# Kernel tuning notes

Hardware: AMD Instinct MI355X
Metric: run time of the kernel (lower is better)

Reference implementation:

```python
import jax, jax.numpy as jnp
import numpy as np

TOPK = 64
MAX_STEP = 3


def gru_cell(x, h, wih, whh, bih, bhh):
    # torch.nn.GRUCell math
    gi = x @ wih.T + bih
    gh = h @ whh.T + bhh
    i_r, i_z, i_n = jnp.split(gi, 3, axis=-1)
    h_r, h_z, h_n = jnp.split(gh, 3, axis=-1)
    r = jax.nn.sigmoid(i_r + h_r)
    z = jax.nn.sigmoid(i_z + h_z)
    n = jnp.tanh(i_n + r * h_n)
    return (1.0 - z) * n + z * h


def t_gruq_forward(query_head, support_rel_all, cos_rel_all, edge_matrix, rel_w, wih, whh, bih, bhh):
    B = query_head.shape[0]
    E = rel_w.shape[1]
    sub_cos = cos_rel_all[support_rel_all]  # [S, R] relation-score rows for support rels

    tree_node_list, tree_node_emb = [], []
    parent_index_list, parent_node_list = [], []
    rel_all_list, rel_b_list = [], []

    current = query_head[:, None]  # [B, 1]
    for step in range(1, MAX_STEP + 1):
        cand = edge_matrix[current]              # [B, nc, nei, 2]
        cand_ent = cand[..., 0]                  # [B, nc, nei]
        cand_rel = cand[..., 1]
        nc, nei = cand_ent.shape[1], cand_ent.shape[2]

        # max over support relations of cos_rel_all[s, r]
        score = sub_cos[:, cand_rel].max(axis=0)           # [B, nc, nei]
        flat = score.reshape(B, -1)                        # [B, nc*nei]
        k = min(TOPK, flat.shape[-1])
        next_scores, next_act = jax.lax.top_k(flat, k)     # [B, k]

        # parent = ceil((next_act+1)/nei) - 1 == next_act // nei
        parent = next_act // nei                           # [B, k]
        aim_ent = jnp.take_along_axis(cand_ent.reshape(B, -1), next_act, axis=1)
        aim_rel = jnp.take_along_axis(cand_rel.reshape(B, -1), next_act, axis=1)
        rel_b_list.append(aim_rel)

        x = rel_w[aim_rel].reshape(-1, E)                  # [B*k, E]
        if step == 1:
            h = jnp.zeros_like(x)
            parent_node_list.append(jnp.broadcast_to(query_head[:, None], (B, k)))
        else:
            h = jnp.take_along_axis(tree_node_emb[step - 2], parent[:, :, None], axis=1).reshape(-1, E)
            parent_node_list.append(jnp.take_along_axis(tree_node_list[step - 2], parent, axis=1))
            parent_index_list.append(parent.astype(jnp.float32))
            rel_all_list.append(jnp.take_along_axis(rel_b_list[step - 2], parent, axis=1))
            if step == MAX_STEP:
                parent_index_list.append(jnp.broadcast_to(jnp.arange(k, dtype=jnp.float32)[None, :], (B, k)))
                rel_all_list.append(aim_rel)
        emb = gru_cell(x, h, wih, whh, bih, bhh).reshape(B, k, E)
        tree_node_emb.append(emb)
        tree_node_list.append(aim_ent)
        current = aim_ent

    tree_node = jnp.stack(tree_node_list, axis=1)          # [B, 3, k]
    tree_emb_all = jnp.stack(tree_node_emb, axis=1)        # [B, 3, k, E]
    parent_index = jnp.stack(parent_index_list, axis=1)    # [B, 3, k]
    parent_node = jnp.stack(parent_node_list, axis=1)      # [B, 3, k]
    aim_rel_all = jnp.stack(rel_all_list, axis=1)          # [B, 3, k]
    return tree_node, tree_emb_all, parent_index, parent_node, aim_rel_all


def setup_inputs() -> dict:
    key = jax.random.key(0)
    ks = jax.random.split(key, 9)
    B, N_ENT, NEI, R, E, S = 512, 50000, 64, 200, 128, 16
    return {
        "query_head": jax.random.randint(ks[0], (B,), 0, N_ENT, dtype=jnp.int32),
        "support_rel_all": jax.random.randint(ks[1], (S,), 0, R, dtype=jnp.int32),
        "cos_rel_all": jax.random.normal(ks[2], (R, R), dtype=jnp.float32),
        "edge_matrix": jax.random.randint(ks[3], (N_ENT, NEI, 2), 0, R, dtype=jnp.int32),
        "rel_w": jax.random.normal(ks[4], (R, E), dtype=jnp.float32) * 0.1,
        "wih": jax.random.normal(ks[5], (3 * E, E), dtype=jnp.float32) * 0.1,
        "whh": jax.random.normal(ks[6], (3 * E, E), dtype=jnp.float32) * 0.1,
        "bih": jax.random.normal(ks[7], (3 * E,), dtype=jnp.float32) * 0.1,
        "bhh": jax.random.normal(ks[8], (3 * E,), dtype=jnp.float32) * 0.1,
    }


def reference(query_head, support_rel_all, cos_rel_all, edge_matrix, rel_w, wih, whh, bih, bhh):
    return t_gruq_forward(query_head, support_rel_all, cos_rel_all, edge_matrix, rel_w, wih, whh, bih, bhh)
```

## Files before the change

kernel.cpp:

```cpp
#include <hip/hip_runtime.h>
#include <hip/hip_bf16.h>
#include <math.h>

#define E 128
#define NEI 64
#define THREE_E 384
#define H2BS 136

typedef __attribute__((ext_vector_type(8))) short short8;
typedef __attribute__((ext_vector_type(4))) short short4v;
typedef __attribute__((ext_vector_type(4))) float f32x4;

__device__ __forceinline__ float sig_(float x) { return 1.0f / (1.0f + __expf(-x)); }
__device__ __forceinline__ float tanh_(float x) {
    float ax = fabsf(x);
    float e = __expf(-2.0f * ax);
    float r = (1.0f - e) / (1.0f + e);
    return copysignf(r, x);
}
__device__ __forceinline__ short bf16_(float x) {
    __hip_bfloat16 h = __float2bfloat16(x);
    return __builtin_bit_cast(short, h);
}

__global__ __launch_bounds__(512) void kAB(
    const int* __restrict__ support, const float* __restrict__ cosr,
    int* __restrict__ rank, int S, int R,
    const float* __restrict__ rel_w, const float* __restrict__ wih,
    const float* __restrict__ bih, float* __restrict__ G,
    const float* __restrict__ whh, const float* __restrict__ bhh,
    float* __restrict__ emb1, float* __restrict__ GH1,
    short* __restrict__ wpack) {
    int blk = blockIdx.x, t = threadIdx.x;
    __shared__ float sm[256];
    __shared__ float grow[THREE_E];
    if (blk < R) {
        int r = blk;
        if (t < E) sm[t] = rel_w[(size_t)r * E + t];
        __syncthreads();
        if (t < THREE_E) {
            float acc = bih[t];
            const float4* w4 = (const float4*)(wih + (size_t)t * E);
#pragma unroll 8
            for (int k = 0; k < E / 4; ++k) {
                float4 wv = w4[k];
                acc += sm[4 * k] * wv.x + sm[4 * k + 1] * wv.y + sm[4 * k + 2] * wv.z +
                       sm[4 * k + 3] * wv.w;
            }
            G[(size_t)r * THREE_E + t] = acc;
            grow[t] = acc;
        }
        __syncthreads();
        if (t < E) {
            float rr = sig_(grow[t] + bhh[t]);
            float zz = sig_(grow[E + t] + bhh[E + t]);
            float nn = tanh_(grow[2 * E + t] + rr * bhh[2 * E + t]);
            float h = (1.0f - zz) * nn;
            sm[t] = h;
            emb1[(size_t)r * E + t] = h;
        }
        __syncthreads();
        if (t < THREE_E) {
            float acc = bhh[t];
            const float4* w4 = (const float4*)(whh + (size_t)t * E);
#pragma unroll 8
            for (int k = 0; k < E / 4; ++k) {
                float4 wv = w4[k];
                acc += sm[4 * k] * wv.x + sm[4 * k + 1] * wv.y + sm[4 * k + 2] * wv.z +
                       sm[4 * k + 3] * wv.w;
            }
            GH1[(size_t)r * THREE_E + t] = acc;
        }
    } else if (blk < R + 96) {
        int idx = (blk - R) * 512 + t;
        int i = idx & 7, l = (idx >> 3) & 63, kt = (idx >> 9) & 3, ct = idx >> 11;
        int er = ct * 16 + (l & 15);
        int k = kt * 32 + (l >> 4) * 8 + i;
        wpack[idx] = bf16_(whh[(size_t)er * E + k]);
    } else {
        if (t < 256) {
            float v = -INFINITY;
            if (t < R)
                for (int s = 0; s < S; ++s) v = fmaxf(v, cosr[support[s] * R + t]);
            sm[t] = v;
        }
        __syncthreads();
        if (t < 256) {
            int rk = 0;
            if (t < R) {
                float v = sm[t];
                for (int r2 = 0; r2 < R; ++r2) {
                    float u = sm[r2];
                    rk += (u > v) || (u == v && r2 < t);
                }
            }
            rank[t] = rk;
        }
    }
}

__global__ __launch_bounds__(512, 6) void k_main(
    const int* __restrict__ query, const int2* __restrict__ edge,
    const int* __restrict__ rank, const float* __restrict__ G,
    const float* __restrict__ GH1, const float* __restrict__ emb1,
    const short* __restrict__ wpack, const float* __restrict__ bhh,
    float* __restrict__ o_tree, float* __restrict__ o_emb,
    float* __restrict__ o_pidx, float* __restrict__ o_pnode,
    float* __restrict__ o_rel) {
    int b = blockIdx.x, t = threadIdx.x;
    __shared__ int rankL[256];
    __shared__ int pe[64], prl[64], npe[64], nprl[64];
    __shared__ int hist[256];
    __shared__ int list[4096];
    __shared__ int win_p[64], win_rel[64], win_prel[64];
    __shared__ int s_c, s_lcnt;
    __shared__ __align__(16) short h2b[64][H2BS];

    const int* edge_i = (const int*)edge;
    if (t < 256) rankL[t] = rank[t];
    int qh = query[b];
    int e1x = 0, e1y = 0;
    if (t < 64) {
        int2 pr = edge[(size_t)qh * NEI + t];
        e1x = pr.x; e1y = pr.y;
    }
    __syncthreads();
    if (t < 64) list[t] = rankL[e1y] * 64 + t;
    __syncthreads();
    if (t < 64) {
        int mykey = list[t], pos = 0;
#pragma unroll
        for (int u = 0; u < 64; ++u) pos += (list[u] < mykey);
        pe[pos] = e1x;
        prl[pos] = e1y;
    }
    if (t < 256) hist[t] = 0;
    if (t == 0) s_lcnt = 0;
    __syncthreads();

    int p0 = t >> 6, n0 = t & 63;
    int rl2[8];
#pragma unroll
    for (int u = 0; u < 8; ++u)
        rl2[u] = edge_i[((size_t)pe[p0 + 8 * u] * NEI + n0) * 2 + 1];
    if (t < 64) {
        o_tree[(b * 3 + 0) * 64 + t] = (float)pe[t];
        o_pnode[(b * 3 + 0) * 64 + t] = (float)qh;
    }
    {
        int j = t >> 3, q = t & 7;
        const float4* src = (const float4*)(emb1 + (size_t)prl[j] * E) + q * 4;
        float4* dst = (float4*)(o_emb + ((size_t)(b * 3 + 0) * 64 + j) * E) + q * 4;
#pragma unroll
        for (int v = 0; v < 4; ++v) dst[v] = src[v];
    }
#pragma unroll
    for (int u = 0; u < 8; ++u) {
        rl2[u] = rankL[rl2[u]];
        atomicAdd(&hist[rl2[u]], 1);
    }
    __syncthreads();
    if (t < 64) {
        int base = 0, c = 255;
        for (int r4 = 0; r4 < 4; ++r4) {
            int sc = hist[r4 * 64 + t];
#pragma unroll
            for (int d = 1; d < 64; d <<= 1) {
                int o = __shfl_up(sc, d, 64);
                if (t >= d) sc += o;
            }
            unsigned long long m = __ballot(base + sc >= 64);
            if (m) { c = r4 * 64 + __ffsll(m) - 1; break; }
            base += __shfl(sc, 63, 64);
        }
        if (t == 0) s_c = c;
    }
    __syncthreads();
    {
        int c = s_c;
#pragma unroll
        for (int u = 0; u < 8; ++u)
            if (rl2[u] <= c) {
                int pos = atomicAdd(&s_lcnt, 1);
                list[pos] = (rl2[u] << 12) | (t + 512 * u);
            }
    }
    __syncthreads();
    int lcnt = s_lcnt;
    if (t < 8 && lcnt + t < 4096) list[lcnt + t] = 0x7fffffff;
    if (t < 256) hist[t] = 0;
    __syncthreads();
    {
        int lp = (lcnt + 7) & ~7;
        for (int e = t; e < lcnt; e += 512) {
            int key = list[e], ord = 0;
            for (int f = 0; f < lp; f += 8)
#pragma unroll
                for (int g = 0; g < 8; ++g) ord += (list[f + g] < key);
            if (ord < 64) {
                int i = key & 4095, p = i >> 6, n = i & 63;
                int2 c2 = edge[(size_t)pe[p] * NEI + n];
                win_rel[ord] = c2.y; win_p[ord] = p; win_prel[ord] = prl[p];
                npe[ord] = c2.x; nprl[ord] = c2.y;
                o_tree[(b * 3 + 1) * 64 + ord] = (float)c2.x;
                o_pnode[(b * 3 + 1) * 64 + ord] = (float)pe[p];
                o_pidx[(b * 3 + 0) * 64 + ord] = (float)p;
                o_rel[(b * 3 + 0) * 64 + ord] = (float)prl[p];
            }
        }
    }
    if (t == 0) s_lcnt = 0;
    __syncthreads();

    int rl3[8];
#pragma unroll
    for (int u = 0; u < 8; ++u)
        rl3[u] = edge_i[((size_t)npe[p0 + 8 * u] * NEI + n0) * 2 + 1];

    {
        int j = t >> 3, q = t & 7;
        int rel = win_rel[j], pr = win_prel[j];
        const float4* Gr = (const float4*)(G + (size_t)rel * THREE_E);
        const float4* Hr = (const float4*)(GH1 + (size_t)pr * THREE_E);
        const float4* h1 = (const float4*)(emb1 + (size_t)pr * E);
        float4* dstg = (float4*)(o_emb + ((size_t)(b * 3 + 1) * 64 + j) * E);
#pragma unroll
        for (int v = 0; v < 4; ++v) {
            int cv = q * 4 + v;
            float4 gr = Gr[cv], gz = Gr[32 + cv], gn = Gr[64 + cv];
            float4 hr = Hr[cv], hz = Hr[32 + cv], hn = Hr[64 + cv];
            float4 h = h1[cv];
            float4 res;
            { float rr = sig_(gr.x + hr.x), zz = sig_(gz.x + hz.x);
              float nn = tanh_(gn.x + rr * hn.x); res.x = (1.0f - zz) * nn + zz * h.x; }
            { float rr = sig_(gr.y + hr.y), zz = sig_(gz.y + hz.y);
              float nn = tanh_(gn.y + rr * hn.y); res.y = (1.0f - zz) * nn + zz * h.y; }
            { float rr = sig_(gr.z + hr.z), zz = sig_(gz.z + hz.z);
              float nn = tanh_(gn.z + rr * hn.z); res.z = (1.0f - zz) * nn + zz * h.z; }
            { float rr = sig_(gr.w + hr.w), zz = sig_(gz.w + hz.w);
              float nn = tanh_(gn.w + rr * hn.w); res.w = (1.0f - zz) * nn + zz * h.w; }
            dstg[cv] = res;
            short4v hb = {bf16_(res.x), bf16_(res.y), bf16_(res.z), bf16_(res.w)};
            *(short4v*)&h2b[j][cv * 4] = hb;
        }
    }
#pragma unroll
    for (int u = 0; u < 8; ++u) {
        rl3[u] = rankL[rl3[u]];
        atomicAdd(&hist[rl3[u]], 1);
    }
    __syncthreads();
    if (t < 64) {
        int base = 0, c = 255;
        for (int r4 = 0; r4 < 4; ++r4) {
            int sc = hist[r4 * 64 + t];
#pragma unroll
            for (int d = 1; d < 64; d <<= 1) {
                int o = __shfl_up(sc, d, 64);
                if (t >= d) sc += o;
            }
            unsigned long long m = __ballot(base + sc >= 64);
            if (m) { c = r4 * 64 + __ffsll(m) - 1; break; }
            base += __shfl(sc, 63, 64);
        }
        if (t == 0) s_c = c;
    }
    __syncthreads();
    {
        int c = s_c;
#pragma unroll
        for (int u = 0; u < 8; ++u)
            if (rl3[u] <= c) {
                int pos = atomicAdd(&s_lcnt, 1);
                list[pos] = (rl3[u] << 12) | (t + 512 * u);
            }
    }
    __syncthreads();
    lcnt = s_lcnt;
    if (t < 8 && lcnt + t < 4096) list[lcnt + t] = 0x7fffffff;
    __syncthreads();
    {
        int lp = (lcnt + 7) & ~7;
        for (int e = t; e < lcnt; e += 512) {
            int key = list[e], ord = 0;
            for (int f = 0; f < lp; f += 8)
#pragma unroll
                for (int g = 0; g < 8; ++g) ord += (list[f + g] < key);
            if (ord < 64) {
                int i = key & 4095, p = i >> 6, n = i & 63;
                int2 c2 = edge[(size_t)npe[p] * NEI + n];
                win_rel[ord] = c2.y; win_p[ord] = p;
                o_tree[(b * 3 + 2) * 64 + ord] = (float)c2.x;
                o_pnode[(b * 3 + 2) * 64 + ord] = (float)npe[p];
                o_pidx[(b * 3 + 1) * 64 + ord] = (float)p;
                o_rel[(b * 3 + 1) * 64 + ord] = (float)nprl[p];
                o_rel[(b * 3 + 2) * 64 + ord] = (float)c2.y;
            }
        }
    }
    if (t < 64) o_pidx[(b * 3 + 2) * 64 + t] = (float)t;
    __syncthreads();

    {
        int lane = t & 63, w = t >> 6;
        int e = w * 16 + (lane & 15);
        float b_r = bhh[e], b_z = bhh[E + e], b_n = bhh[2 * E + e];
#pragma unroll
        for (int half = 0; half < 2; ++half) {
            f32x4 acc[3][2];
#pragma unroll
            for (int g = 0; g < 3; ++g)
#pragma unroll
                for (int rt = 0; rt < 2; ++rt) acc[g][rt] = (f32x4){0.f, 0.f, 0.f, 0.f};
            int pw[2];
#pragma unroll
            for (int rt = 0; rt < 2; ++rt)
                pw[rt] = win_p[(half * 2 + rt) * 16 + (lane & 15)];
#pragma unroll
            for (int kt = 0; kt < 4; ++kt) {
                short8 af[2];
#pragma unroll
                for (int rt = 0; rt < 2; ++rt)
                    af[rt] = *(const short8*)&h2b[pw[rt]][(lane >> 4) * 8 + kt * 32];
#pragma unroll
                for (int g = 0; g < 3; ++g) {
                    short8 bf =
                        *(const short8*)(wpack + ((size_t)((g * 8 + w) * 4 + kt) * 64 + lane) * 8);
#pragma unroll
                    for (int rt = 0; rt < 2; ++rt)
                        acc[g][rt] = __builtin_amdgcn_mfma_f32_16x16x32_bf16(
                            af[rt], bf, acc[g][rt], 0, 0, 0);
                }
            }
#pragma unroll
            for (int rt = 0; rt < 2; ++rt)
#pragma unroll
                for (int reg = 0; reg < 4; ++reg) {
                    int j = (half * 2 + rt) * 16 + (lane >> 4) * 4 + reg;
                    int rel = win_rel[j];
                    float rr = sig_(G[(size_t)rel * THREE_E + e] + acc[0][rt][reg] + b_r);
                    float zz = sig_(G[(size_t)rel * THREE_E + E + e] + acc[1][rt][reg] + b_z);
                    float nn = tanh_(G[(size_t)rel * THREE_E + 2 * E + e] +
                                     rr * (acc[2][rt][reg] + b_n));
                    int p = win_p[j];
                    float h = __bfloat162float(__builtin_bit_cast(__hip_bfloat16, h2b[p][e]));
                    o_emb[((size_t)(b * 3 + 2) * 64 + j) * E + e] = (1.0f - zz) * nn + zz * h;
                }
        }
    }
}

extern "C" void kernel_launch(void* const* d_in, const int* in_sizes, int n_in,
                              void* d_out, int out_size, void* d_ws, size_t ws_size,
                              hipStream_t stream) {
    const int* query = (const int*)d_in[0];
    const int* support = (const int*)d_in[1];
    const float* cosr = (const float*)d_in[2];
    const int2* edge = (const int2*)d_in[3];
    const float* rel_w = (const float*)d_in[4];
    const float* wih = (const float*)d_in[5];
    const float* whh = (const float*)d_in[6];
    const float* bih = (const float*)d_in[7];
    const float* bhh = (const float*)d_in[8];
    int B = in_sizes[0];
    int S = in_sizes[1];
    int R = in_sizes[4] / E;

    float* out = (float*)d_out;
    size_t o_tree = 0;
    size_t o_emb = (size_t)B * 3 * 64;
    size_t o_pidx = o_emb + (size_t)B * 3 * 64 * E;
    size_t o_pnode = o_pidx + (size_t)B * 3 * 64;
    size_t o_rel = o_pnode + (size_t)B * 3 * 64;

    char* ws = (char*)d_ws;
    int* rank = (int*)ws;      ws += 256 * 4;
    float* G = (float*)ws;     ws += (size_t)R * THREE_E * 4;
    float* emb1 = (float*)ws;  ws += (size_t)R * E * 4;
    float* GH1 = (float*)ws;   ws += (size_t)R * THREE_E * 4;
    short* wpack = (short*)ws; ws += (size_t)24 * 4 * 64 * 8 * 2;

    kAB<<<R + 96 + 1, 512, 0, stream>>>(support, cosr, rank, S, R, rel_w, wih, bih,
                                        G, whh, bhh, emb1, GH1, wpack);
    k_main<<<B, 512, 0, stream>>>(query, edge, rank, G, GH1, emb1, wpack, bhh,
                                  out + o_tree, out + o_emb, out + o_pidx,
                                  out + o_pnode, out + o_rel);
}
```

Before: 57.59 us.

## Fuse precompute and main kernels with a grid-wide atomic barrier

Merges the table-precompute kernel into the main tree-search kernel. Blocks below R build the G/emb1/GH1 tables and blocks in the next 96 pack the weights. Every block recomputes the relation ranking locally and then waits on a global atomic counter before it reads the shared tables. The step-1 embedding copy and the step-2 GRU move after that barrier, so step-1 and step-2 top-k selection overlaps with table construction. The aim is to remove a kernel launch and the serialization between the two kernels. In exchange it needs all 512 blocks co-resident to avoid deadlock, adds a memset and repeats the ranking work in every block.

```diff
diff --git a/kernel.cpp b/kernel.cpp
--- a/kernel.cpp
+++ b/kernel.cpp
@@ -23,20 +23,40 @@
     return __builtin_bit_cast(short, h);
 }
 
-__global__ __launch_bounds__(512) void kAB(
-    const int* __restrict__ support, const float* __restrict__ cosr,
-    int* __restrict__ rank, int S, int R,
+__global__ __launch_bounds__(512, 6) void k_all(
+    const int* __restrict__ query, const int* __restrict__ support,
+    const float* __restrict__ cosr, const int2* __restrict__ edge,
     const float* __restrict__ rel_w, const float* __restrict__ wih,
-    const float* __restrict__ bih, float* __restrict__ G,
-    const float* __restrict__ whh, const float* __restrict__ bhh,
-    float* __restrict__ emb1, float* __restrict__ GH1,
-    short* __restrict__ wpack) {
-    int blk = blockIdx.x, t = threadIdx.x;
-    __shared__ float sm[256];
-    __shared__ float grow[THREE_E];
-    if (blk < R) {
-        int r = blk;
-        if (t < E) sm[t] = rel_w[(size_t)r * E + t];
+    const float* __restrict__ whh, const float* __restrict__ bih,
+    const float* __restrict__ bhh,
+    float* __restrict__ G, float* __restrict__ emb1, float* __restrict__ GH1,
+    short* __restrict__ wpack, int* __restrict__ bar,
+    float* __restrict__ o_tree, float* __restrict__ o_emb,
+    float* __restrict__ o_pidx, float* __restrict__ o_pnode,
+    float* __restrict__ o_rel, int R, int S, int NB) {
+    int b = blockIdx.x, t = threadIdx.x;
+    __shared__ int rankL[256];
+    __shared__ int pe[64], prl[64], prl0[64], npe[64], nprl[64];
+    __shared__ int hist[256];
+    __shared__ int list[4096];
+    __shared__ int win_p[64], win_rel[64], win_prel[64];
+    __shared__ int s_c, s_lcnt;
+    __shared__ __align__(16) short h2b[64][H2BS];
+
+    const int* edge_i = (const int*)edge;
+    float* smf = (float*)&h2b[0][0];
+    float* grow = smf + 128;
+    float* mxc = smf + 512;
+
+    int qh = query[b];
+    int e1x = 0, e1y = 0;
+    if (t < 64) {
+        int2 pr = edge[(size_t)qh * NEI + t];
+        e1x = pr.x; e1y = pr.y;
+    }
+
+    if (b < R) {
+        if (t < E) smf[t] = rel_w[(size_t)b * E + t];
         __syncthreads();
         if (t < THREE_E) {
             float acc = bih[t];
@@ -44,10 +64,10 @@
 #pragma unroll 8
             for (int k = 0; k < E / 4; ++k) {
                 float4 wv = w4[k];
-                acc += sm[4 * k] * wv.x + sm[4 * k + 1] * wv.y + sm[4 * k + 2] * wv.z +
-                       sm[4 * k + 3] * wv.w;
-            }
-            G[(size_t)r * THREE_E + t] = acc;
+                acc += smf[4 * k] * wv.x + smf[4 * k + 1] * wv.y + smf[4 * k + 2] * wv.z +
+                       smf[4 * k + 3] * wv.w;
+            }
+            G[(size_t)b * THREE_E + t] = acc;
             grow[t] = acc;
         }
         __syncthreads();
@@ -56,8 +76,8 @@
             float zz = sig_(grow[E + t] + bhh[E + t]);
             float nn = tanh_(grow[2 * E + t] + rr * bhh[2 * E + t]);
             float h = (1.0f - zz) * nn;
-            sm[t] = h;
-            emb1[(size_t)r * E + t] = h;
+            smf[t] = h;
+            emb1[(size_t)b * E + t] = h;
         }
         __syncthreads();
         if (t < THREE_E) {
@@ -66,65 +86,40 @@
 #pragma unroll 8
             for (int k = 0; k < E / 4; ++k) {
                 float4 wv = w4[k];
-                acc += sm[4 * k] * wv.x + sm[4 * k + 1] * wv.y + sm[4 * k + 2] * wv.z +
-                       sm[4 * k + 3] * wv.w;
-            }
-            GH1[(size_t)r * THREE_E + t] = acc;
-        }
-    } else if (blk < R + 96) {
-        int idx = (blk - R) * 512 + t;
+                acc += smf[4 * k] * wv.x + smf[4 * k + 1] * wv.y + smf[4 * k + 2] * wv.z +
+                       smf[4 * k + 3] * wv.w;
+            }
+            GH1[(size_t)b * THREE_E + t] = acc;
+        }
+    } else if (b < R + 96) {
+        int idx = (b - R) * 512 + t;
         int i = idx & 7, l = (idx >> 3) & 63, kt = (idx >> 9) & 3, ct = idx >> 11;
-        int er = ct * 16 + (l & 15);
-        int k = kt * 32 + (l >> 4) * 8 + i;
-        wpack[idx] = bf16_(whh[(size_t)er * E + k]);
-    } else {
-        if (t < 256) {
-            float v = -INFINITY;
-            if (t < R)
-                for (int s = 0; s < S; ++s) v = fmaxf(v, cosr[support[s] * R + t]);
-            sm[t] = v;
-        }
-        __syncthreads();
-        if (t < 256) {
-            int rk = 0;
-            if (t < R) {
-                float v = sm[t];
-                for (int r2 = 0; r2 < R; ++r2) {
-                    float u = sm[r2];
-                    rk += (u > v) || (u == v && r2 < t);
-                }
-            }
-            rank[t] = rk;
-        }
-    }
-}
-
-__global__ __launch_bounds__(512, 6) void k_main(
-    const int* __restrict__ query, const int2* __restrict__ edge,
-    const int* __restrict__ rank, const float* __restrict__ G,
-    const float* __restrict__ GH1, const float* __restrict__ emb1,
-    const short* __restrict__ wpack, const float* __restrict__ bhh,
-    float* __restrict__ o_tree, float* __restrict__ o_emb,
-    float* __restrict__ o_pidx, float* __restrict__ o_pnode,
-    float* __restrict__ o_rel) {
-    int b = blockIdx.x, t = threadIdx.x;
-    __shared__ int rankL[256];
-    __shared__ int pe[64], prl[64], npe[64], nprl[64];
-    __shared__ int hist[256];
-    __shared__ int list[4096];
-    __shared__ int win_p[64], win_rel[64], win_prel[64];
-    __shared__ int s_c, s_lcnt;
-    __shared__ __align__(16) short h2b[64][H2BS];
-
-    const int* edge_i = (const int*)edge;
-    if (t < 256) rankL[t] = rank[t];
-    int qh = query[b];
-    int e1x = 0, e1y = 0;
-    if (t < 64) {
-        int2 pr = edge[(size_t)qh * NEI + t];
-        e1x = pr.x; e1y = pr.y;
-    }
-    __syncthreads();
+        wpack[idx] = bf16_(whh[(size_t)(ct * 16 + (l & 15)) * E + kt * 32 + (l >> 4) * 8 + i]);
+    }
+    __syncthreads();
+
+    if (t < 256) {
+        float v = -INFINITY;
+        if (t < R)
+            for (int s = 0; s < S; ++s) v = fmaxf(v, cosr[support[s] * R + t]);
+        mxc[t] = v;
+    }
+    __syncthreads();
+    if (t < 256) {
+        int rk = 0;
+        if (t < R) {
+            float v = mxc[t];
+            for (int r2 = 0; r2 < R; ++r2) {
+                float u = mxc[r2];
+                rk += (u > v) || (u == v && r2 < t);
+            }
+        }
+        rankL[t] = rk;
+        hist[t] = 0;
+    }
+    if (t == 0) s_lcnt = 0;
+    __syncthreads();
+
     if (t < 64) list[t] = rankL[e1y] * 64 + t;
     __syncthreads();
     if (t < 64) {
@@ -134,26 +129,18 @@
         pe[pos] = e1x;
         prl[pos] = e1y;
     }
-    if (t < 256) hist[t] = 0;
-    if (t == 0) s_lcnt = 0;
-    __syncthreads();
+    __syncthreads();
+    if (t < 64) {
+        prl0[t] = prl[t];
+        o_tree[(b * 3 + 0) * 64 + t] = (float)pe[t];
+        o_pnode[(b * 3 + 0) * 64 + t] = (float)qh;
+    }
 
     int p0 = t >> 6, n0 = t & 63;
     int rl2[8];
 #pragma unroll
     for (int u = 0; u < 8; ++u)
         rl2[u] = edge_i[((size_t)pe[p0 + 8 * u] * NEI + n0) * 2 + 1];
-    if (t < 64) {
-        o_tree[(b * 3 + 0) * 64 + t] = (float)pe[t];
-        o_pnode[(b * 3 + 0) * 64 + t] = (float)qh;
-    }
-    {
-        int j = t >> 3, q = t & 7;
-        const float4* src = (const float4*)(emb1 + (size_t)prl[j] * E) + q * 4;
-        float4* dst = (float4*)(o_emb + ((size_t)(b * 3 + 0) * 64 + j) * E) + q * 4;
-#pragma unroll
-        for (int v = 0; v < 4; ++v) dst[v] = src[v];
-    }
 #pragma unroll
     for (int u = 0; u < 8; ++u) {
         rl2[u] = rankL[rl2[u]];
@@ -211,11 +198,32 @@
     }
     if (t == 0) s_lcnt = 0;
     __syncthreads();
+    if (t < 64) { pe[t] = npe[t]; prl[t] = nprl[t]; }
+    __syncthreads();
 
     int rl3[8];
 #pragma unroll
     for (int u = 0; u < 8; ++u)
-        rl3[u] = edge_i[((size_t)npe[p0 + 8 * u] * NEI + n0) * 2 + 1];
+        rl3[u] = edge_i[((size_t)pe[p0 + 8 * u] * NEI + n0) * 2 + 1];
+
+    __syncthreads();
+    if (t == 0) {
+        __threadfence();
+        atomicAdd(bar, 1);
+        while (__hip_atomic_load(bar, __ATOMIC_ACQUIRE, __HIP_MEMORY_SCOPE_AGENT) < NB) {
+            __builtin_amdgcn_s_sleep(8);
+        }
+        __threadfence();
+    }
+    __syncthreads();
+
+    {
+        int j = t >> 3, q = t & 7;
+        const float4* src = (const float4*)(emb1 + (size_t)prl0[j] * E) + q * 4;
+        float4* dst = (float4*)(o_emb + ((size_t)(b * 3 + 0) * 64 + j) * E) + q * 4;
+#pragma unroll
+        for (int v = 0; v < 4; ++v) dst[v] = src[v];
+    }
 
     {
         int j = t >> 3, q = t & 7;
@@ -244,6 +252,7 @@
             *(short4v*)&h2b[j][cv * 4] = hb;
         }
     }
+
 #pragma unroll
     for (int u = 0; u < 8; ++u) {
         rl3[u] = rankL[rl3[u]];
@@ -288,12 +297,12 @@
                 for (int g = 0; g < 8; ++g) ord += (list[f + g] < key);
             if (ord < 64) {
                 int i = key & 4095, p = i >> 6, n = i & 63;
-                int2 c2 = edge[(size_t)npe[p] * NEI + n];
+                int2 c2 = edge[(size_t)pe[p] * NEI + n];
                 win_rel[ord] = c2.y; win_p[ord] = p;
                 o_tree[(b * 3 + 2) * 64 + ord] = (float)c2.x;
-                o_pnode[(b * 3 + 2) * 64 + ord] = (float)npe[p];
+                o_pnode[(b * 3 + 2) * 64 + ord] = (float)pe[p];
                 o_pidx[(b * 3 + 1) * 64 + ord] = (float)p;
-                o_rel[(b * 3 + 1) * 64 + ord] = (float)nprl[p];
+                o_rel[(b * 3 + 1) * 64 + ord] = (float)prl[p];
                 o_rel[(b * 3 + 2) * 64 + ord] = (float)c2.y;
             }
         }
@@ -374,15 +383,15 @@
     size_t o_rel = o_pnode + (size_t)B * 3 * 64;
 
     char* ws = (char*)d_ws;
-    int* rank = (int*)ws;      ws += 256 * 4;
+    int* bar = (int*)ws;       ws += 256;
     float* G = (float*)ws;     ws += (size_t)R * THREE_E * 4;
     float* emb1 = (float*)ws;  ws += (size_t)R * E * 4;
     float* GH1 = (float*)ws;   ws += (size_t)R * THREE_E * 4;
     short* wpack = (short*)ws; ws += (size_t)24 * 4 * 64 * 8 * 2;
 
-    kAB<<<R + 96 + 1, 512, 0, stream>>>(support, cosr, rank, S, R, rel_w, wih, bih,
-                                        G, whh, bhh, emb1, GH1, wpack);
-    k_main<<<B, 512, 0, stream>>>(query, edge, rank, G, GH1, emb1, wpack, bhh,
-                                  out + o_tree, out + o_emb, out + o_pidx,
-                                  out + o_pnode, out + o_rel);
+    hipMemsetAsync(bar, 0, sizeof(int), stream);
+    k_all<<<B, 512, 0, stream>>>(query, support, cosr, edge, rel_w, wih, whh, bih, bhh,
+                                 G, emb1, GH1, wpack, bar,
+                                 out + o_tree, out + o_emb, out + o_pidx,
+                                 out + o_pnode, out + o_rel, R, S, B);
 }
```

Measured after the change: 138.0 us. +139.6%, slower.

## Double k_main block size to 1024 threads, halving per-thread work

Applied to the files above, without the earlier changes.

Launches k_main with 1024 threads per block instead of 512, so each thread handles 4 candidate edges instead of 8 and half as many float4 copies. In the GRU MFMA stage the two row halves now go to separate wave groups rather than a sequential loop. The step-2 parent arrays are copied into pe/prl before step 3, which adds one extra barrier. The aim is more memory-level parallelism and latency hiding for the gather-heavy top-k stages, at the risk of lower occupancy and costlier block-wide syncs with larger blocks.

```diff
diff --git a/kernel.cpp b/kernel.cpp
--- a/kernel.cpp
+++ b/kernel.cpp
@@ -74,9 +74,7 @@
     } else if (blk < R + 96) {
         int idx = (blk - R) * 512 + t;
         int i = idx & 7, l = (idx >> 3) & 63, kt = (idx >> 9) & 3, ct = idx >> 11;
-        int er = ct * 16 + (l & 15);
-        int k = kt * 32 + (l >> 4) * 8 + i;
-        wpack[idx] = bf16_(whh[(size_t)er * E + k]);
+        wpack[idx] = bf16_(whh[(size_t)(ct * 16 + (l & 15)) * E + kt * 32 + (l >> 4) * 8 + i]);
     } else {
         if (t < 256) {
             float v = -INFINITY;
@@ -99,7 +97,7 @@
     }
 }
 
-__global__ __launch_bounds__(512, 6) void k_main(
+__global__ __launch_bounds__(1024, 8) void k_main(
     const int* __restrict__ query, const int2* __restrict__ edge,
     const int* __restrict__ rank, const float* __restrict__ G,
     const float* __restrict__ GH1, const float* __restrict__ emb1,
@@ -139,23 +137,23 @@
     __syncthreads();
 
     int p0 = t >> 6, n0 = t & 63;
-    int rl2[8];
-#pragma unroll
-    for (int u = 0; u < 8; ++u)
-        rl2[u] = edge_i[((size_t)pe[p0 + 8 * u] * NEI + n0) * 2 + 1];
+    int rl2[4];
+#pragma unroll
+    for (int u = 0; u < 4; ++u)
+        rl2[u] = edge_i[((size_t)pe[p0 + 16 * u] * NEI + n0) * 2 + 1];
     if (t < 64) {
         o_tree[(b * 3 + 0) * 64 + t] = (float)pe[t];
         o_pnode[(b * 3 + 0) * 64 + t] = (float)qh;
     }
     {
-        int j = t >> 3, q = t & 7;
-        const float4* src = (const float4*)(emb1 + (size_t)prl[j] * E) + q * 4;
-        float4* dst = (float4*)(o_emb + ((size_t)(b * 3 + 0) * 64 + j) * E) + q * 4;
-#pragma unroll
-        for (int v = 0; v < 4; ++v) dst[v] = src[v];
-    }
-#pragma unroll
-    for (int u = 0; u < 8; ++u) {
+        int j = t >> 4, q = t & 15;
+        const float4* src = (const float4*)(emb1 + (size_t)prl[j] * E) + q * 2;
+        float4* dst = (float4*)(o_emb + ((size_t)(b * 3 + 0) * 64 + j) * E) + q * 2;
+        dst[0] = src[0];
+        dst[1] = src[1];
+    }
+#pragma unroll
+    for (int u = 0; u < 4; ++u) {
         rl2[u] = rankL[rl2[u]];
         atomicAdd(&hist[rl2[u]], 1);
     }
@@ -179,10 +177,10 @@
     {
         int c = s_c;
 #pragma unroll
-        for (int u = 0; u < 8; ++u)
+        for (int u = 0; u < 4; ++u)
             if (rl2[u] <= c) {
                 int pos = atomicAdd(&s_lcnt, 1);
-                list[pos] = (rl2[u] << 12) | (t + 512 * u);
+                list[pos] = (rl2[u] << 12) | (t + 1024 * u);
             }
     }
     __syncthreads();
@@ -192,7 +190,7 @@
     __syncthreads();
     {
         int lp = (lcnt + 7) & ~7;
-        for (int e = t; e < lcnt; e += 512) {
+        for (int e = t; e < lcnt; e += 1024) {
             int key = list[e], ord = 0;
             for (int f = 0; f < lp; f += 8)
 #pragma unroll
@@ -211,22 +209,24 @@
     }
     if (t == 0) s_lcnt = 0;
     __syncthreads();
-
-    int rl3[8];
-#pragma unroll
-    for (int u = 0; u < 8; ++u)
-        rl3[u] = edge_i[((size_t)npe[p0 + 8 * u] * NEI + n0) * 2 + 1];
-
-    {
-        int j = t >> 3, q = t & 7;
+    if (t < 64) { pe[t] = npe[t]; prl[t] = nprl[t]; }
+    __syncthreads();
+
+    int rl3[4];
+#pragma unroll
+    for (int u = 0; u < 4; ++u)
+        rl3[u] = edge_i[((size_t)pe[p0 + 16 * u] * NEI + n0) * 2 + 1];
+
+    {
+        int j = t >> 4, q = t & 15;
         int rel = win_rel[j], pr = win_prel[j];
         const float4* Gr = (const float4*)(G + (size_t)rel * THREE_E);
         const float4* Hr = (const float4*)(GH1 + (size_t)pr * THREE_E);
         const float4* h1 = (const float4*)(emb1 + (size_t)pr * E);
         float4* dstg = (float4*)(o_emb + ((size_t)(b * 3 + 1) * 64 + j) * E);
 #pragma unroll
-        for (int v = 0; v < 4; ++v) {
-            int cv = q * 4 + v;
+        for (int v = 0; v < 2; ++v) {
+            int cv = q * 2 + v;
             float4 gr = Gr[cv], gz = Gr[32 + cv], gn = Gr[64 + cv];
             float4 hr = Hr[cv], hz = Hr[32 + cv], hn = Hr[64 + cv];
             float4 h = h1[cv];
@@ -245,7 +245,7 @@
         }
     }
 #pragma unroll
-    for (int u = 0; u < 8; ++u) {
+    for (int u = 0; u < 4; ++u) {
         rl3[u] = rankL[rl3[u]];
         atomicAdd(&hist[rl3[u]], 1);
     }
@@ -269,10 +269,10 @@
     {
         int c = s_c;
 #pragma unroll
-        for (int u = 0; u < 8; ++u)
+        for (int u = 0; u < 4; ++u)
             if (rl3[u] <= c) {
                 int pos = atomicAdd(&s_lcnt, 1);
-                list[pos] = (rl3[u] << 12) | (t + 512 * u);
+                list[pos] = (rl3[u] << 12) | (t + 1024 * u);
             }
     }
     __syncthreads();
@@ -281,19 +281,19 @@
     __syncthreads();
     {
         int lp = (lcnt + 7) & ~7;
-        for (int e = t; e < lcnt; e += 512) {
+        for (int e = t; e < lcnt; e += 1024) {
             int key = list[e], ord = 0;
             for (int f = 0; f < lp; f += 8)
 #pragma unroll
                 for (int g = 0; g < 8; ++g) ord += (list[f + g] < key);
             if (ord < 64) {
                 int i = key & 4095, p = i >> 6, n = i & 63;
-                int2 c2 = edge[(size_t)npe[p] * NEI + n];
+                int2 c2 = edge[(size_t)pe[p] * NEI + n];
                 win_rel[ord] = c2.y; win_p[ord] = p;
                 o_tree[(b * 3 + 2) * 64 + ord] = (float)c2.x;
-                o_pnode[(b * 3 + 2) * 64 + ord] = (float)npe[p];
+                o_pnode[(b * 3 + 2) * 64 + ord] = (float)pe[p];
                 o_pidx[(b * 3 + 1) * 64 + ord] = (float)p;
-                o_rel[(b * 3 + 1) * 64 + ord] = (float)nprl[p];
+                o_rel[(b * 3 + 1) * 64 + ord] = (float)prl[p];
                 o_rel[(b * 3 + 2) * 64 + ord] = (float)c2.y;
             }
         }
@@ -303,50 +303,48 @@
 
     {
         int lane = t & 63, w = t >> 6;
-        int e = w * 16 + (lane & 15);
+        int half = w >> 3, ww = w & 7;
+        int e = ww * 16 + (lane & 15);
         float b_r = bhh[e], b_z = bhh[E + e], b_n = bhh[2 * E + e];
-#pragma unroll
-        for (int half = 0; half < 2; ++half) {
-            f32x4 acc[3][2];
-#pragma unroll
-            for (int g = 0; g < 3; ++g)
-#pragma unroll
-                for (int rt = 0; rt < 2; ++rt) acc[g][rt] = (f32x4){0.f, 0.f, 0.f, 0.f};
-            int pw[2];
+        f32x4 acc[3][2];
+#pragma unroll
+        for (int g = 0; g < 3; ++g)
+#pragma unroll
+            for (int rt = 0; rt < 2; ++rt) acc[g][rt] = (f32x4){0.f, 0.f, 0.f, 0.f};
+        int pw[2];
+#pragma unroll
+        for (int rt = 0; rt < 2; ++rt)
+            pw[rt] = win_p[(half * 2 + rt) * 16 + (lane & 15)];
+#pragma unroll
+        for (int kt = 0; kt < 4; ++kt) {
+            short8 af[2];
 #pragma unroll
             for (int rt = 0; rt < 2; ++rt)
-                pw[rt] = win_p[(half * 2 + rt) * 16 + (lane & 15)];
-#pragma unroll
-            for (int kt = 0; kt < 4; ++kt) {
-                short8 af[2];
+                af[rt] = *(const short8*)&h2b[pw[rt]][(lane >> 4) * 8 + kt * 32];
+#pragma unroll
+            for (int g = 0; g < 3; ++g) {
+                short8 bf =
+                    *(const short8*)(wpack + ((size_t)((g * 8 + ww) * 4 + kt) * 64 + lane) * 8);
 #pragma unroll
                 for (int rt = 0; rt < 2; ++rt)
-                    af[rt] = *(const short8*)&h2b[pw[rt]][(lane >> 4) * 8 + kt * 32];
-#pragma unroll
-                for (int g = 0; g < 3; ++g) {
-                    short8 bf =
-                        *(const short8*)(wpack + ((size_t)((g * 8 + w) * 4 + kt) * 64 + lane) * 8);
-#pragma unroll
-                    for (int rt = 0; rt < 2; ++rt)
-                        acc[g][rt] = __builtin_amdgcn_mfma_f32_16x16x32_bf16(
-                            af[rt], bf, acc[g][rt], 0, 0, 0);
-                }
-            }
-#pragma unroll
-            for (int rt = 0; rt < 2; ++rt)
-#pragma unroll
-                for (int reg = 0; reg < 4; ++reg) {
-                    int j = (half * 2 + rt) * 16 + (lane >> 4) * 4 + reg;
-                    int rel = win_rel[j];
-                    float rr = sig_(G[(size_t)rel * THREE_E + e] + acc[0][rt][reg] + b_r);
-                    float zz = sig_(G[(size_t)rel * THREE_E + E + e] + acc[1][rt][reg] + b_z);
-                    float nn = tanh_(G[(size_t)rel * THREE_E + 2 * E + e] +
-                                     rr * (acc[2][rt][reg] + b_n));
-                    int p = win_p[j];
-                    float h = __bfloat162float(__builtin_bit_cast(__hip_bfloat16, h2b[p][e]));
-                    o_emb[((size_t)(b * 3 + 2) * 64 + j) * E + e] = (1.0f - zz) * nn + zz * h;
-                }
-        }
+                    acc[g][rt] = __builtin_amdgcn_mfma_f32_16x16x32_bf16(
+                        af[rt], bf, acc[g][rt], 0, 0, 0);
+            }
+        }
+#pragma unroll
+        for (int rt = 0; rt < 2; ++rt)
+#pragma unroll
+            for (int reg = 0; reg < 4; ++reg) {
+                int jj = (half * 2 + rt) * 16 + (lane >> 4) * 4 + reg;
+                int rel = win_rel[jj];
+                float rr = sig_(G[(size_t)rel * THREE_E + e] + acc[0][rt][reg] + b_r);
+                float zz = sig_(G[(size_t)rel * THREE_E + E + e] + acc[1][rt][reg] + b_z);
+                float nn = tanh_(G[(size_t)rel * THREE_E + 2 * E + e] +
+                                 rr * (acc[2][rt][reg] + b_n));
+                int p = win_p[jj];
+                float h = __bfloat162float(__builtin_bit_cast(__hip_bfloat16, h2b[p][e]));
+                o_emb[((size_t)(b * 3 + 2) * 64 + jj) * E + e] = (1.0f - zz) * nn + zz * h;
+            }
     }
 }
 
@@ -382,7 +380,7 @@
 
     kAB<<<R + 96 + 1, 512, 0, stream>>>(support, cosr, rank, S, R, rel_w, wih, bih,
                                         G, whh, bhh, emb1, GH1, wpack);
-    k_main<<<B, 512, 0, stream>>>(query, edge, rank, G, GH1, emb1, wpack, bhh,
-                                  out + o_tree, out + o_emb, out + o_pidx,
-                                  out + o_pnode, out + o_rel);
-}
+    k_main<<<B, 1024, 0, stream>>>(query, edge, rank, G, GH1, emb1, wpack, bhh,
+                                   out + o_tree, out + o_emb, out + o_pidx,
+                                   out + o_pnode, out + o_rel);
+}
```

Measured after the change: 46.96 us (median of 2 runs). -18.5%, faster.
